# Kernel tuning notes

Hardware: AMD Instinct MI355X
Metric: run time of the kernel (lower is better)

The kernel has to match this reference:

```python
import jax, jax.numpy as jnp
import numpy as np

N, C_IN, H, W = 32, 128, 56, 56
C_OUT, K = 256, 3
STRIDE = (1, 1)
PAD = (1, 1)


def setup_inputs() -> dict:
    key = jax.random.key(0)
    kx, kw = jax.random.split(key)
    x = jax.random.normal(kx, (N, C_IN, H, W), dtype=jnp.float32)
    k = 1.0 / np.sqrt(C_IN * K * K)
    kernels = jax.random.uniform(kw, (C_OUT, C_IN, K, K), dtype=jnp.float32) * (2 * k) - k
    return {"x": x, "kernels": kernels}


def reference(x, kernels):
    # Equivalent to the im2col + matmul conv in the source (zero padding,
    # stride 1, no bias added in the original forward).
    out = jax.lax.conv_general_dilated(
        x, kernels,
        window_strides=STRIDE,
        padding=[(PAD[0], PAD[0]), (PAD[1], PAD[1])],
        dimension_numbers=("NCHW", "OIHW", "NCHW"),
    )
    return out  # (N, C_OUT, H_out, W_out)
```

## Files before the change

kernel.cpp:

```cpp
#include <hip/hip_runtime.h>


#define CIN   128
#define COUT  256
#define HWID  56
#define IMG   (HWID*HWID)
#define NIMG  32
#define XP    32
#define XCH   (232*XP)

typedef __attribute__((ext_vector_type(8))) short short8;
typedef __attribute__((ext_vector_type(4))) float float4v;

__device__ __forceinline__ unsigned short f2bf(float f) {
    unsigned int u = __builtin_bit_cast(unsigned int, f);
    u += 0x7FFFu + ((u >> 16) & 1u);
    return (unsigned short)(u >> 16);
}

__global__ __launch_bounds__(256) void prep_w_kernel(const float* __restrict__ w,
                                                     unsigned short* __restrict__ W2) {
    int o = blockIdx.x * 256 + threadIdx.x;
    int ci_lo = o & 31;
    int co    = (o >> 5) & 255;
    int s     = o >> 13;
    int ci_hi = s / 9;
    int r9    = s - ci_hi * 9;
    W2[o] = f2bf(w[(co * CIN + ci_hi * 32 + ci_lo) * 9 + r9]);
}

__global__ __launch_bounds__(256, 2)
void conv_mfma_kernel(const float* __restrict__ x,
                      const unsigned short* __restrict__ W2,
                      float* __restrict__ out) {
    __shared__ __align__(16) unsigned short Xs[4 * XCH];

    const int tid  = threadIdx.x;
    const int lane = tid & 63;
    const int wv   = tid >> 6;
    const int l15  = lane & 15;
    const int quad = lane >> 4;

    const int pt    = (blockIdx.x & 7) * 112 + (blockIdx.x >> 3);
    const int n_img = pt / 28;
    const int h0    = (pt % 28) * 2;

    {
        const int h     = h0 - 1 + wv;
        const int wpix  = lane - 1;
        const bool vald = ((unsigned)h < 56u) & ((unsigned)wpix < 56u);
        const float* xcol = x + ((long)n_img * CIN) * IMG + h * HWID + wpix;
        const int rc = wv * 58 + lane;

        if (lane < 58) {
            #pragma unroll
            for (int c8 = 0; c8 < 16; ++c8) {
                short8 o = (short8){0,0,0,0,0,0,0,0};
                if (vald) {
                    float v0 = xcol[(c8*8 + 0) * IMG];
                    float v1 = xcol[(c8*8 + 1) * IMG];
                    float v2 = xcol[(c8*8 + 2) * IMG];
                    float v3 = xcol[(c8*8 + 3) * IMG];
                    float v4 = xcol[(c8*8 + 4) * IMG];
                    float v5 = xcol[(c8*8 + 5) * IMG];
                    float v6 = xcol[(c8*8 + 6) * IMG];
                    float v7 = xcol[(c8*8 + 7) * IMG];
                    unsigned int* op = (unsigned int*)&o;
                    op[0] = (unsigned int)f2bf(v0) | ((unsigned int)f2bf(v1) << 16);
                    op[1] = (unsigned int)f2bf(v2) | ((unsigned int)f2bf(v3) << 16);
                    op[2] = (unsigned int)f2bf(v4) | ((unsigned int)f2bf(v5) << 16);
                    op[3] = (unsigned int)f2bf(v6) | ((unsigned int)f2bf(v7) << 16);
                }
                *(short8*)(&Xs[(c8 >> 2) * XCH + rc * XP + (c8 & 3) * 8]) = o;
            }
        }
    }
    __syncthreads();

    int boff[7];
    #pragma unroll
    for (int n = 0; n < 7; ++n) {
        int p    = n * 16 + l15;
        int prow = (p >= 56) ? 1 : 0;
        int pcol = p - prow * 56;
        boff[n]  = (prow * 58 + pcol) * XP + quad * 8;
    }

    const unsigned short* wbase = W2 + (wv * 64 + l15) * 32 + quad * 8;

    float4v acc[4][7];
    #pragma unroll
    for (int m = 0; m < 4; ++m)
        #pragma unroll
        for (int n = 0; n < 7; ++n)
            acc[m][n] = (float4v){0.f, 0.f, 0.f, 0.f};

    short8 a[4], an[4];
    #pragma unroll
    for (int m = 0; m < 4; ++m)
        a[m] = *(const short8*)(wbase + m * 512);

    #pragma unroll
    for (int ci_hi = 0; ci_hi < 4; ++ci_hi) {
        #pragma unroll
        for (int khw = 0; khw < 9; ++khw) {
            const int step = ci_hi * 9 + khw;
            const int kh = khw / 3, kw = khw - (khw / 3) * 3;
            if (step < 35) {
                #pragma unroll
                for (int m = 0; m < 4; ++m)
                    an[m] = *(const short8*)(wbase + (step + 1) * 8192 + m * 512);
            }
            short8 bfr[7];
            #pragma unroll
            for (int n = 0; n < 7; ++n)
                bfr[n] = *(const short8*)(&Xs[ci_hi * XCH + boff[n] + (kh * 58 + kw) * XP]);
            #pragma unroll
            for (int m = 0; m < 4; ++m)
                #pragma unroll
                for (int n = 0; n < 7; ++n)
                    acc[m][n] = __builtin_amdgcn_mfma_f32_16x16x32_bf16(a[m], bfr[n], acc[m][n], 0, 0, 0);
            if (step < 35) {
                #pragma unroll
                for (int m = 0; m < 4; ++m)
                    a[m] = an[m];
            }
        }
    }

    float* obase = out + (long)n_img * (COUT * IMG) + h0 * HWID;
    #pragma unroll
    for (int m = 0; m < 4; ++m) {
        #pragma unroll
        for (int r = 0; r < 4; ++r) {
            int co = wv * 64 + m * 16 + quad * 4 + r;
            float* orow = obase + (long)co * IMG;
            #pragma unroll
            for (int n = 0; n < 7; ++n)
                orow[n * 16 + l15] = acc[m][n][r];
        }
    }
}

extern "C" void kernel_launch(void* const* d_in, const int* in_sizes, int n_in,
                              void* d_out, int out_size, void* d_ws, size_t ws_size,
                              hipStream_t stream) {
    const float* x  = (const float*)d_in[0];
    const float* wt = (const float*)d_in[1];
    float* out = (float*)d_out;

    unsigned short* W2 = (unsigned short*)d_ws;

    prep_w_kernel<<<(COUT * CIN * 9) / 256, 256, 0, stream>>>(wt, W2);
    conv_mfma_kernel<<<NIMG * 28, 256, 0, stream>>>(x, W2, out);
}
```

Measured before the change: 183.5 us.

## Interleave channels per pixel row in LDS and double-buffer B fragments

```diff
diff --git a/kernel.cpp b/kernel.cpp
--- a/kernel.cpp
+++ b/kernel.cpp
@@ -6,8 +6,7 @@
 #define HWID  56
 #define IMG   (HWID*HWID)
 #define NIMG  32
-#define XP    32
-#define XCH   (232*XP)
+#define RSTR  136
 
 typedef __attribute__((ext_vector_type(8))) short short8;
 typedef __attribute__((ext_vector_type(4))) float float4v;
@@ -33,7 +32,7 @@
 void conv_mfma_kernel(const float* __restrict__ x,
                       const unsigned short* __restrict__ W2,
                       float* __restrict__ out) {
-    __shared__ __align__(16) unsigned short Xs[4 * XCH];
+    __shared__ __align__(16) unsigned short Xs[232 * RSTR];
 
     const int tid  = threadIdx.x;
     const int lane = tid & 63;
@@ -71,7 +70,7 @@
                     op[2] = (unsigned int)f2bf(v4) | ((unsigned int)f2bf(v5) << 16);
                     op[3] = (unsigned int)f2bf(v6) | ((unsigned int)f2bf(v7) << 16);
                 }
-                *(short8*)(&Xs[(c8 >> 2) * XCH + rc * XP + (c8 & 3) * 8]) = o;
+                *(short8*)(&Xs[rc * RSTR + c8 * 8]) = o;
             }
         }
     }
@@ -83,7 +82,7 @@
         int p    = n * 16 + l15;
         int prow = (p >= 56) ? 1 : 0;
         int pcol = p - prow * 56;
-        boff[n]  = (prow * 58 + pcol) * XP + quad * 8;
+        boff[n]  = (prow * 58 + pcol) * RSTR + quad * 8;
     }
 
     const unsigned short* wbase = W2 + (wv * 64 + l15) * 32 + quad * 8;
@@ -95,36 +94,47 @@
         for (int n = 0; n < 7; ++n)
             acc[m][n] = (float4v){0.f, 0.f, 0.f, 0.f};
 
-    short8 a[4], an[4];
+    short8 a[4], an[4], b0[7], b1[7];
     #pragma unroll
     for (int m = 0; m < 4; ++m)
         a[m] = *(const short8*)(wbase + m * 512);
+    #pragma unroll
+    for (int n = 0; n < 7; ++n)
+        b0[n] = *(const short8*)(&Xs[boff[n]]);
 
     #pragma unroll
-    for (int ci_hi = 0; ci_hi < 4; ++ci_hi) {
-        #pragma unroll
-        for (int khw = 0; khw < 9; ++khw) {
-            const int step = ci_hi * 9 + khw;
-            const int kh = khw / 3, kw = khw - (khw / 3) * 3;
-            if (step < 35) {
+    for (int s = 0; s < 36; ++s) {
+        if (s < 35) {
+            const int s1     = s + 1;
+            const int ci_hi1 = s1 / 9;
+            const int khw1   = s1 % 9;
+            const int kh1 = khw1 / 3, kw1 = khw1 - kh1 * 3;
+            const int xoff1  = (kh1 * 58 + kw1) * RSTR + ci_hi1 * 32;
+            if (s & 1) {
                 #pragma unroll
-                for (int m = 0; m < 4; ++m)
-                    an[m] = *(const short8*)(wbase + (step + 1) * 8192 + m * 512);
+                for (int n = 0; n < 7; ++n)
+                    b0[n] = *(const short8*)(&Xs[boff[n] + xoff1]);
+            } else {
+                #pragma unroll
+                for (int n = 0; n < 7; ++n)
+                    b1[n] = *(const short8*)(&Xs[boff[n] + xoff1]);
             }
-            short8 bfr[7];
-            #pragma unroll
-            for (int n = 0; n < 7; ++n)
-                bfr[n] = *(const short8*)(&Xs[ci_hi * XCH + boff[n] + (kh * 58 + kw) * XP]);
             #pragma unroll
             for (int m = 0; m < 4; ++m)
-                #pragma unroll
-                for (int n = 0; n < 7; ++n)
-                    acc[m][n] = __builtin_amdgcn_mfma_f32_16x16x32_bf16(a[m], bfr[n], acc[m][n], 0, 0, 0);
-            if (step < 35) {
-                #pragma unroll
-                for (int m = 0; m < 4; ++m)
-                    a[m] = an[m];
+                an[m] = *(const short8*)(wbase + s1 * 8192 + m * 512);
+        }
+        #pragma unroll
+        for (int m = 0; m < 4; ++m) {
+            #pragma unroll
+            for (int n = 0; n < 7; ++n) {
+                const short8 bf = (s & 1) ? b1[n] : b0[n];
+                acc[m][n] = __builtin_amdgcn_mfma_f32_16x16x32_bf16(a[m], bf, acc[m][n], 0, 0, 0);
             }
+        }
+        if (s < 35) {
+            #pragma unroll
+            for (int m = 0; m < 4; ++m)
+                a[m] = an[m];
         }
     }
 
```

Result: no change. 181.1 us (-1.3%).

## Interleave channels per pixel row in LDS and batch two K-steps of B loads

Applied to the files above, without the earlier changes.

```diff
diff --git a/kernel.cpp b/kernel.cpp
--- a/kernel.cpp
+++ b/kernel.cpp
@@ -6,8 +6,7 @@
 #define HWID  56
 #define IMG   (HWID*HWID)
 #define NIMG  32
-#define XP    32
-#define XCH   (232*XP)
+#define RSTR  136
 
 typedef __attribute__((ext_vector_type(8))) short short8;
 typedef __attribute__((ext_vector_type(4))) float float4v;
@@ -33,7 +32,7 @@
 void conv_mfma_kernel(const float* __restrict__ x,
                       const unsigned short* __restrict__ W2,
                       float* __restrict__ out) {
-    __shared__ __align__(16) unsigned short Xs[4 * XCH];
+    __shared__ __align__(16) unsigned short Xs[232 * RSTR];
 
     const int tid  = threadIdx.x;
     const int lane = tid & 63;
@@ -44,6 +43,13 @@
     const int pt    = (blockIdx.x & 7) * 112 + (blockIdx.x >> 3);
     const int n_img = pt / 28;
     const int h0    = (pt % 28) * 2;
+
+    const unsigned short* wbase = W2 + (wv * 64 + l15) * 32 + quad * 8;
+
+    short8 a[4], an[4];
+    #pragma unroll
+    for (int m = 0; m < 4; ++m)
+        a[m] = *(const short8*)(wbase + m * 512);
 
     {
         const int h     = h0 - 1 + wv;
@@ -71,7 +77,7 @@
                     op[2] = (unsigned int)f2bf(v4) | ((unsigned int)f2bf(v5) << 16);
                     op[3] = (unsigned int)f2bf(v6) | ((unsigned int)f2bf(v7) << 16);
                 }
-                *(short8*)(&Xs[(c8 >> 2) * XCH + rc * XP + (c8 & 3) * 8]) = o;
+                *(short8*)(&Xs[rc * RSTR + c8 * 8]) = o;
             }
         }
     }
@@ -83,10 +89,8 @@
         int p    = n * 16 + l15;
         int prow = (p >= 56) ? 1 : 0;
         int pcol = p - prow * 56;
-        boff[n]  = (prow * 58 + pcol) * XP + quad * 8;
+        boff[n]  = (prow * 58 + pcol) * RSTR + quad * 8;
     }
-
-    const unsigned short* wbase = W2 + (wv * 64 + l15) * 32 + quad * 8;
 
     float4v acc[4][7];
     #pragma unroll
@@ -95,36 +99,46 @@
         for (int n = 0; n < 7; ++n)
             acc[m][n] = (float4v){0.f, 0.f, 0.f, 0.f};
 
-    short8 a[4], an[4];
     #pragma unroll
-    for (int m = 0; m < 4; ++m)
-        a[m] = *(const short8*)(wbase + m * 512);
-
-    #pragma unroll
-    for (int ci_hi = 0; ci_hi < 4; ++ci_hi) {
+    for (int s2 = 0; s2 < 18; ++s2) {
+        const int s0 = 2 * s2;
+        short8 b[14];
         #pragma unroll
-        for (int khw = 0; khw < 9; ++khw) {
-            const int step = ci_hi * 9 + khw;
-            const int kh = khw / 3, kw = khw - (khw / 3) * 3;
-            if (step < 35) {
-                #pragma unroll
-                for (int m = 0; m < 4; ++m)
-                    an[m] = *(const short8*)(wbase + (step + 1) * 8192 + m * 512);
-            }
-            short8 bfr[7];
+        for (int half = 0; half < 2; ++half) {
+            const int s     = s0 + half;
+            const int ci_hi = s / 9;
+            const int khw   = s % 9;
+            const int kh = khw / 3, kw = khw - kh * 3;
+            const int xoff = (kh * 58 + kw) * RSTR + ci_hi * 32;
             #pragma unroll
             for (int n = 0; n < 7; ++n)
-                bfr[n] = *(const short8*)(&Xs[ci_hi * XCH + boff[n] + (kh * 58 + kw) * XP]);
+                b[half * 7 + n] = *(const short8*)(&Xs[boff[n] + xoff]);
+        }
+        #pragma unroll
+        for (int m = 0; m < 4; ++m)
+            an[m] = *(const short8*)(wbase + (s0 + 1) * 8192 + m * 512);
+        #pragma unroll
+        for (int m = 0; m < 4; ++m)
+            #pragma unroll
+            for (int n = 0; n < 7; ++n)
+                acc[m][n] = __builtin_amdgcn_mfma_f32_16x16x32_bf16(a[m], b[n], acc[m][n], 0, 0, 0);
+        #pragma unroll
+        for (int m = 0; m < 4; ++m)
+            a[m] = an[m];
+        if (s2 < 17) {
             #pragma unroll
             for (int m = 0; m < 4; ++m)
-                #pragma unroll
-                for (int n = 0; n < 7; ++n)
-                    acc[m][n] = __builtin_amdgcn_mfma_f32_16x16x32_bf16(a[m], bfr[n], acc[m][n], 0, 0, 0);
-            if (step < 35) {
-                #pragma unroll
-                for (int m = 0; m < 4; ++m)
-                    a[m] = an[m];
-            }
+                an[m] = *(const short8*)(wbase + (s0 + 2) * 8192 + m * 512);
+        }
+        #pragma unroll
+        for (int m = 0; m < 4; ++m)
+            #pragma unroll
+            for (int n = 0; n < 7; ++n)
+                acc[m][n] = __builtin_amdgcn_mfma_f32_16x16x32_bf16(a[m], b[7 + n], acc[m][n], 0, 0, 0);
+        if (s2 < 17) {
+            #pragma unroll
+            for (int m = 0; m < 4; ++m)
+                a[m] = an[m];
         }
     }
 
```

Result: no change. 181.2 us (-1.2%).
